# Performance work log

Measured on AMD Instinct MI355X. Metric: run time of the kernel, lower is better.

## Reference

```python
import jax, jax.numpy as jnp
import numpy as np

K = 32            # number of stocks to select (init kwarg k)
TEMP = 1.0        # initial_temperature, no annealing applied
EPS = 1e-10
MASK_SUB = 10000.0


def setup_inputs() -> dict:
    key = jax.random.key(0)
    k1, k2 = jax.random.split(key)
    scores = jax.random.normal(k1, (4096, 8192), dtype=jnp.float32)
    u = jax.random.uniform(k2, (4096, 8192), dtype=jnp.float32)
    return {"scores": scores, "u": u}


def reference(scores, u):
    # gumbel noise exactly as torch: -log(-log(rand + eps) + eps)
    gumbel = -jnp.log(-jnp.log(u + EPS) + EPS)
    perturbed = (scores + gumbel) / TEMP

    # iterative soft top-k: k rounds of softmax + suppress selected mass
    def step(carry, _):
        soft_mask, remaining = carry
        s = jax.nn.softmax(remaining, axis=-1)
        return (soft_mask + s, remaining - s * MASK_SUB), None

    (soft_mask, _), _ = jax.lax.scan(
        step, (jnp.zeros_like(scores), perturbed), None, length=K)

    # hard top-k mask from raw scores
    _, idx = jax.lax.top_k(scores, K)                      # (B, K)
    B = scores.shape[0]
    hard_mask = jnp.zeros_like(scores).at[
        jnp.arange(B)[:, None], idx].set(1.0)

    # straight-through: forward == hard_mask, backward through soft_mask
    return hard_mask - jax.lax.stop_gradient(soft_mask) + soft_mask
```

## Files before the change

kernel.cpp:

```cpp
#include <hip/hip_runtime.h>


constexpr int ROWS = 4096;
constexpr int COLS = 8192;
constexpr int TPB  = 256;
constexpr int VPT  = COLS / TPB / 4;
constexpr int KSEL = 32;
constexpr int CAP  = 1024;

__device__ __forceinline__ unsigned f2key(float f) {
    unsigned b = __float_as_uint(f);
    return (b & 0x80000000u) ? ~b : (b | 0x80000000u);
}

__global__ __launch_bounds__(TPB, 4) void topk_mask_kernel(
        const float* __restrict__ scores, float* __restrict__ out) {
    const int tid = threadIdx.x;
    const size_t base = (size_t)blockIdx.x * COLS;
    const float4* __restrict__ src = reinterpret_cast<const float4*>(scores + base);
    float4*       __restrict__ dst = reinterpret_cast<float4*>(out + base);

    __shared__ __align__(16) unsigned       ckey[CAP];
    __shared__ __align__(16) unsigned short cidx[CAP];
    __shared__ unsigned bitmap[COLS / 32];
    __shared__ unsigned cnt;

    float4 vv[VPT];
#pragma unroll
    for (int j = 0; j < VPT; ++j) vv[j] = src[tid + j * TPB];

    reinterpret_cast<uint4*>(ckey)[tid] = make_uint4(0, 0, 0, 0);
    bitmap[tid] = 0;
    if (tid == 0) cnt = 0;
    __syncthreads();

    unsigned C;
    for (int attempt = 0; ; ++attempt) {
        const float tval = (attempt == 0) ? 2.0f
                         : (attempt == 1) ? 0.0f
                         : (attempt == 2) ? -2.0f : -3.4e38f;
        const unsigned tkey = f2key(tval);
#pragma unroll
        for (int j = 0; j < VPT; ++j) {
            const float f[4] = {vv[j].x, vv[j].y, vv[j].z, vv[j].w};
#pragma unroll
            for (int c = 0; c < 4; ++c) {
                const unsigned k = f2key(f[c]);
                if (k > tkey) {
                    const unsigned p = atomicAdd(&cnt, 1u);
                    if (p < CAP) {
                        ckey[p] = k;
                        cidx[p] = (unsigned short)(4 * (tid + j * TPB) + c);
                    }
                }
            }
        }
        __syncthreads();
        C = cnt;
        if (C >= (unsigned)KSEL || attempt >= 3) break;
        __syncthreads();
        if (tid == 0) cnt = 0;
        reinterpret_cast<uint4*>(ckey)[tid] = make_uint4(0, 0, 0, 0);
        __syncthreads();
    }
    if (C > (unsigned)CAP) C = CAP;

    {
        const unsigned C4 = (C + 3) >> 2;
        const uint4*   ck4 = reinterpret_cast<const uint4*>(ckey);
        const ushort4* ci4 = reinterpret_cast<const ushort4*>(cidx);
        for (unsigned q = tid; q < C; q += TPB) {
            const unsigned kq = ckey[q];
            const unsigned iq = cidx[q];
            unsigned r = 0;
            for (unsigned p = 0; p < C4; ++p) {
                const uint4   kk = ck4[p];
                const ushort4 ii = ci4[p];
                r += (kk.x > kq) + (kk.y > kq) + (kk.z > kq) + (kk.w > kq);
                r += (kk.x == kq && ii.x < iq);
                r += (kk.y == kq && ii.y < iq);
                r += (kk.z == kq && ii.z < iq);
                r += (kk.w == kq && ii.w < iq);
            }
            if (r < (unsigned)KSEL)
                atomicOr(&bitmap[iq >> 5], 1u << (iq & 31u));
        }
    }
    __syncthreads();

#pragma unroll
    for (int j = 0; j < VPT; ++j) {
        const unsigned w  = bitmap[(tid >> 3) + 32 * j];
        const unsigned sh = 4u * (tid & 7u);
        float4 o;
        o.x = ((w >> (sh + 0)) & 1u) ? 1.0f : 0.0f;
        o.y = ((w >> (sh + 1)) & 1u) ? 1.0f : 0.0f;
        o.z = ((w >> (sh + 2)) & 1u) ? 1.0f : 0.0f;
        o.w = ((w >> (sh + 3)) & 1u) ? 1.0f : 0.0f;
        dst[tid + j * TPB] = o;
    }
}

extern "C" void kernel_launch(void* const* d_in, const int* in_sizes, int n_in,
                              void* d_out, int out_size, void* d_ws, size_t ws_size,
                              hipStream_t stream) {
    const float* scores = (const float*)d_in[0];
    float* out = (float*)d_out;
    topk_mask_kernel<<<dim3(ROWS), dim3(TPB), 0, stream>>>(scores, out);
}
```

Baseline: 284.8 us.

## Process two rows per block with next-row prefetch and nontemporal stores

Each block now handles two rows and loads the second row's scores into registers while the first row's selection and output run. Rare fallback threshold passes re-read values from global memory instead of registers. Output writes use nontemporal stores to avoid polluting cache. This halves the grid size, which may reduce occupancy and latency hiding on a memory-bound kernel.

```diff
diff --git a/kernel.cpp b/kernel.cpp
--- a/kernel.cpp
+++ b/kernel.cpp
@@ -7,6 +7,10 @@
 constexpr int VPT  = COLS / TPB / 4;
 constexpr int KSEL = 32;
 constexpr int CAP  = 1024;
+constexpr int RPB  = 2;
+constexpr int GRID = ROWS / RPB;
+
+typedef float nfloat4 __attribute__((ext_vector_type(4)));
 
 __device__ __forceinline__ unsigned f2key(float f) {
     unsigned b = __float_as_uint(f);
@@ -15,31 +19,31 @@
 
 __global__ __launch_bounds__(TPB, 4) void topk_mask_kernel(
         const float* __restrict__ scores, float* __restrict__ out) {
-    const int tid = threadIdx.x;
-    const size_t base = (size_t)blockIdx.x * COLS;
-    const float4* __restrict__ src = reinterpret_cast<const float4*>(scores + base);
-    float4*       __restrict__ dst = reinterpret_cast<float4*>(out + base);
+    const int tid  = threadIdx.x;
+    const int row0 = blockIdx.x * RPB;
 
     __shared__ __align__(16) unsigned       ckey[CAP];
     __shared__ __align__(16) unsigned short cidx[CAP];
     __shared__ unsigned bitmap[COLS / 32];
     __shared__ unsigned cnt;
 
-    float4 vv[VPT];
-#pragma unroll
-    for (int j = 0; j < VPT; ++j) vv[j] = src[tid + j * TPB];
-
     reinterpret_cast<uint4*>(ckey)[tid] = make_uint4(0, 0, 0, 0);
     bitmap[tid] = 0;
     if (tid == 0) cnt = 0;
+
+    float4 vv[VPT];
+    {
+        const float4* src0 =
+            reinterpret_cast<const float4*>(scores + (size_t)row0 * COLS);
+#pragma unroll
+        for (int j = 0; j < VPT; ++j) vv[j] = src0[tid + j * TPB];
+    }
     __syncthreads();
 
-    unsigned C;
-    for (int attempt = 0; ; ++attempt) {
-        const float tval = (attempt == 0) ? 2.0f
-                         : (attempt == 1) ? 0.0f
-                         : (attempt == 2) ? -2.0f : -3.4e38f;
-        const unsigned tkey = f2key(tval);
+    for (int r = 0; r < RPB; ++r) {
+        const size_t base = (size_t)(row0 + r) * COLS;
+
+        const unsigned tkey = f2key(2.0f);
 #pragma unroll
         for (int j = 0; j < VPT; ++j) {
             const float f[4] = {vv[j].x, vv[j].y, vv[j].z, vv[j].w};
@@ -55,49 +59,82 @@
                 }
             }
         }
+
+        if (r + 1 < RPB) {
+            const float4* srcn =
+                reinterpret_cast<const float4*>(scores + base + COLS);
+#pragma unroll
+            for (int j = 0; j < VPT; ++j) vv[j] = srcn[tid + j * TPB];
+        }
         __syncthreads();
-        C = cnt;
-        if (C >= (unsigned)KSEL || attempt >= 3) break;
+        unsigned C = cnt;
+
+        if (C < (unsigned)KSEL) {
+            for (int attempt = 1; ; ++attempt) {
+                __syncthreads();
+                if (tid == 0) cnt = 0;
+                reinterpret_cast<uint4*>(ckey)[tid] = make_uint4(0, 0, 0, 0);
+                __syncthreads();
+                const float tval = (attempt == 1) ? 0.0f
+                                 : (attempt == 2) ? -2.0f : -3.4e38f;
+                const unsigned tk = f2key(tval);
+                for (int e = tid; e < COLS; e += TPB) {
+                    const unsigned k = f2key(scores[base + e]);
+                    if (k > tk) {
+                        const unsigned p = atomicAdd(&cnt, 1u);
+                        if (p < CAP) { ckey[p] = k; cidx[p] = (unsigned short)e; }
+                    }
+                }
+                __syncthreads();
+                C = cnt;
+                if (C >= (unsigned)KSEL || attempt >= 3) break;
+            }
+        }
+        if (C > (unsigned)CAP) C = CAP;
+
+        {
+            const unsigned C4  = (C + 3) >> 2;
+            const uint4*   ck4 = reinterpret_cast<const uint4*>(ckey);
+            const ushort4* ci4 = reinterpret_cast<const ushort4*>(cidx);
+            for (unsigned q = tid; q < C; q += TPB) {
+                const unsigned kq = ckey[q];
+                const unsigned iq = cidx[q];
+                unsigned rr = 0;
+                for (unsigned p = 0; p < C4; ++p) {
+                    const uint4   kk = ck4[p];
+                    const ushort4 ii = ci4[p];
+                    rr += (kk.x > kq) + (kk.y > kq) + (kk.z > kq) + (kk.w > kq);
+                    rr += (kk.x == kq && ii.x < iq);
+                    rr += (kk.y == kq && ii.y < iq);
+                    rr += (kk.z == kq && ii.z < iq);
+                    rr += (kk.w == kq && ii.w < iq);
+                }
+                if (rr < (unsigned)KSEL)
+                    atomicOr(&bitmap[iq >> 5], 1u << (iq & 31u));
+            }
+        }
         __syncthreads();
-        if (tid == 0) cnt = 0;
-        reinterpret_cast<uint4*>(ckey)[tid] = make_uint4(0, 0, 0, 0);
-        __syncthreads();
-    }
-    if (C > (unsigned)CAP) C = CAP;
 
-    {
-        const unsigned C4 = (C + 3) >> 2;
-        const uint4*   ck4 = reinterpret_cast<const uint4*>(ckey);
-        const ushort4* ci4 = reinterpret_cast<const ushort4*>(cidx);
-        for (unsigned q = tid; q < C; q += TPB) {
-            const unsigned kq = ckey[q];
-            const unsigned iq = cidx[q];
-            unsigned r = 0;
-            for (unsigned p = 0; p < C4; ++p) {
-                const uint4   kk = ck4[p];
-                const ushort4 ii = ci4[p];
-                r += (kk.x > kq) + (kk.y > kq) + (kk.z > kq) + (kk.w > kq);
-                r += (kk.x == kq && ii.x < iq);
-                r += (kk.y == kq && ii.y < iq);
-                r += (kk.z == kq && ii.z < iq);
-                r += (kk.w == kq && ii.w < iq);
-            }
-            if (r < (unsigned)KSEL)
-                atomicOr(&bitmap[iq >> 5], 1u << (iq & 31u));
+        nfloat4* dst = reinterpret_cast<nfloat4*>(out + base);
+#pragma unroll
+        for (int j = 0; j < VPT; ++j) {
+            const unsigned w  = bitmap[(tid >> 3) + 32 * j];
+            const unsigned sh = 4u * (tid & 7u);
+            nfloat4 o;
+            o.x = ((w >> (sh + 0)) & 1u) ? 1.0f : 0.0f;
+            o.y = ((w >> (sh + 1)) & 1u) ? 1.0f : 0.0f;
+            o.z = ((w >> (sh + 2)) & 1u) ? 1.0f : 0.0f;
+            o.w = ((w >> (sh + 3)) & 1u) ? 1.0f : 0.0f;
+            __builtin_nontemporal_store(o, &dst[tid + j * TPB]);
         }
-    }
-    __syncthreads();
 
-#pragma unroll
-    for (int j = 0; j < VPT; ++j) {
-        const unsigned w  = bitmap[(tid >> 3) + 32 * j];
-        const unsigned sh = 4u * (tid & 7u);
-        float4 o;
-        o.x = ((w >> (sh + 0)) & 1u) ? 1.0f : 0.0f;
-        o.y = ((w >> (sh + 1)) & 1u) ? 1.0f : 0.0f;
-        o.z = ((w >> (sh + 2)) & 1u) ? 1.0f : 0.0f;
-        o.w = ((w >> (sh + 3)) & 1u) ? 1.0f : 0.0f;
-        dst[tid + j * TPB] = o;
+        if (r + 1 < RPB) {
+            __syncthreads();
+            reinterpret_cast<uint4*>(ckey)[tid] = make_uint4(0, 0, 0, 0);
+            bitmap[tid] = 0;
+            if (tid == 0) cnt = 0;
+            __syncthreads();
+        }
     }
 }
 
@@ -106,5 +143,5 @@
                               hipStream_t stream) {
     const float* scores = (const float*)d_in[0];
     float* out = (float*)d_out;
-    topk_mask_kernel<<<dim3(ROWS), dim3(TPB), 0, stream>>>(scores, out);
+    topk_mask_kernel<<<dim3(GRID), dim3(TPB), 0, stream>>>(scores, out);
 }
```

New measurement: 307.2 us. 1.08x slower.
